# Optimization experiments

Hardware: AMD Instinct MI355X
Metric: run time of the kernel (lower is better)

## Reference

```python
import jax, jax.numpy as jnp
import numpy as np

B, N, C, H = 16, 577, 768, 12
D = C // H
BETA = 1.0
KEEP_RATIO = 0.5


def setup_inputs() -> dict:
    key = jax.random.key(0)
    k0, k1, k2, k3 = jax.random.split(key, 4)
    x = jax.random.normal(k0, (B, N, C), dtype=jnp.float32)
    # UCB visit-count buffer, strictly positive as accumulated counts would be
    ucb_count_score = jax.random.uniform(k1, (H, N), dtype=jnp.float32) * 50.0 + 1.0
    Wqkv = jax.random.normal(k2, (3 * C, C), dtype=jnp.float32) * 0.02
    Wproj = jax.random.normal(k3, (C, C), dtype=jnp.float32) * 0.02
    bproj = jnp.zeros((C,), dtype=jnp.float32)
    counter = 60  # > 50 so pruning path is taken
    return {"x": x, "ucb_count_score": ucb_count_score, "Wqkv": Wqkv,
            "Wproj": Wproj, "bproj": bproj, "counter": counter}


def reference(x, ucb_count_score, Wqkv, Wproj, bproj, counter):
    # UCBAttention.forward with pruning_enabled=True, selection_mode='ucb',
    # ucb_update_enabled=True, exclude_cls=True, dropout=0 (eval).
    Bs, Ns, Cs = x.shape
    scale = D ** -0.5
    k_keep = max(1, int((Ns - 1) * KEEP_RATIO))  # _get_k with keep_ratio

    qkv = (x @ Wqkv.T).reshape(Bs, Ns, 3, H, D).transpose(2, 0, 3, 1, 4)  # [3,B,H,N,D]
    q, k, v = qkv[0], qkv[1], qkv[2]
    attn_scores = jnp.einsum('bhqd,bhkd->bhqk', q, k) * scale
    attn_probs = jax.nn.softmax(attn_scores, axis=-1)  # [B,H,N,N]

    # UCB scores over patches (CLS excluded)
    patch_scores = attn_probs[:, :, :, 1:].mean(axis=2)            # [B,H,N-1]
    expl = BETA * jnp.sqrt(jnp.log(counter + 1.0) / (ucb_count_score[:, 1:] + 1e-6))
    ucb_scores = patch_scores + expl[None, :, :]                   # [B,H,N-1]
    global_ucb = ucb_scores.mean(axis=1)                           # [B,N-1]
    _, topk_rel = jax.lax.top_k(global_ucb, k_keep)                # [B,k]
    kept = topk_rel + 1                                            # token indices

    # keep-vector: CLS (0) always kept; mask[i,j] = kept[i] OR kept[j]
    kv_mask = (jnp.zeros((Bs, Ns), attn_probs.dtype)
               .at[jnp.arange(Bs)[:, None], kept].set(1.0)
               .at[:, 0].set(1.0))                                 # [B,N]
    mask = jnp.maximum(kv_mask[:, None, :, None], kv_mask[:, None, None, :])  # [B,1,N,N]

    pruned = attn_probs * mask
    pruned = pruned / (pruned.sum(axis=-1, keepdims=True) + 1e-8)
    context = jnp.einsum('bhqk,bhkd->bhqd', pruned, v)             # [B,H,N,D]

    out = context.transpose(0, 2, 1, 3).reshape(Bs, Ns, Cs) @ Wproj.T + bproj

    # score_delta: +1/B at each kept token column, broadcast over heads
    delta = jnp.zeros((Ns,), jnp.float32).at[kept.reshape(-1)].add(1.0 / Bs)
    score_delta = jnp.broadcast_to(delta[None, :], ucb_count_score.shape)
    return out, score_delta, kept
```

## Files before the change

### kernel.cpp

```cpp
#include <hip/hip_runtime.h>
#include <cstdio>
#include <cstdint>

#define B_    16
#define N_    577
#define C_    768
#define H_    12
#define D_    64
#define KKEEP 288
#define SCALE 0.125f
#define LOG2E 1.4426950408889634f
#define M_TOT (B_ * N_)
#define NKT   24
#define PLROW ((size_t)N_ * 64)

typedef __bf16 bf16x8_t __attribute__((ext_vector_type(8)));
typedef __bf16 bf16x4_t __attribute__((ext_vector_type(4)));
typedef float  f32x4_t  __attribute__((ext_vector_type(4)));
typedef unsigned int u32x4_t __attribute__((ext_vector_type(4)));
typedef unsigned int u32x2_t __attribute__((ext_vector_type(2)));

__device__ __forceinline__ f32x4_t mfma_bf16(bf16x8_t a, bf16x8_t b, f32x4_t c) {
    return __builtin_amdgcn_mfma_f32_16x16x32_bf16(a, b, c, 0, 0, 0);
}

__device__ __forceinline__ void gload16(const ushort* g, ushort* l) {
    __builtin_amdgcn_global_load_lds(
        (const __attribute__((address_space(1))) void*)g,
        (__attribute__((address_space(3))) void*)l, 16, 0, 0);
}
#define VMCNT(n) asm volatile("s_waitcnt vmcnt(" #n ")" ::: "memory")
#define SB() __builtin_amdgcn_sched_barrier(0)

__device__ __forceinline__ int xcd_swz(int bid, int nwg) {
    int q = nwg >> 3, r = nwg & 7;
    int xcd = bid & 7, off = bid >> 3;
    int base = (xcd < r) ? xcd * (q + 1) : r * (q + 1) + (xcd - r) * q;
    return base + off;
}

__device__ __forceinline__ void splitf(float x, unsigned int &hi, unsigned int &lo) {
    unsigned int u = __float_as_uint(x);
    hi = u >> 16;
    float r = x - __uint_as_float(u & 0xffff0000u);
    lo = __float_as_uint(r) >> 16;
}
__device__ __forceinline__ unsigned int bf16rne(float x) {
    unsigned int u = __float_as_uint(x);
    return (u + 0x7fffu + ((u >> 16) & 1u)) >> 16;
}

__global__ __launch_bounds__(256) void pack_tiles_kernel(const float* __restrict__ src,
                                                         ushort* __restrict__ dH,
                                                         ushort* __restrict__ dL,
                                                         int nrows) {
    int tile = blockIdx.x;
    int kt = tile % NKT, mt = tile / NKT;
    int w = threadIdx.x;
    int row = w >> 1, h = w & 1;
    int m = mt * 128 + row;
    int sw = (row >> 1) & 3;
    float f[16];
    if (m < nrows) {
        const float* s = src + (size_t)m * C_ + kt * 32;
        int sa = (2 * h) ^ sw, sb = (2 * h + 1) ^ sw;
        *(float4*)&f[0]  = *(const float4*)(s + sa * 8);
        *(float4*)&f[4]  = *(const float4*)(s + sa * 8 + 4);
        *(float4*)&f[8]  = *(const float4*)(s + sb * 8);
        *(float4*)&f[12] = *(const float4*)(s + sb * 8 + 4);
    } else {
#pragma unroll
        for (int i = 0; i < 16; i++) f[i] = 0.f;
    }
    unsigned hi[16], lo[16];
#pragma unroll
    for (int i = 0; i < 16; i++) splitf(f[i], hi[i], lo[i]);
    u32x4_t h0 = {hi[0] | (hi[1] << 16), hi[2] | (hi[3] << 16),
                  hi[4] | (hi[5] << 16), hi[6] | (hi[7] << 16)};
    u32x4_t h1 = {hi[8] | (hi[9] << 16), hi[10] | (hi[11] << 16),
                  hi[12] | (hi[13] << 16), hi[14] | (hi[15] << 16)};
    u32x4_t l0 = {lo[0] | (lo[1] << 16), lo[2] | (lo[3] << 16),
                  lo[4] | (lo[5] << 16), lo[6] | (lo[7] << 16)};
    u32x4_t l1 = {lo[8] | (lo[9] << 16), lo[10] | (lo[11] << 16),
                  lo[12] | (lo[13] << 16), lo[14] | (lo[15] << 16)};
    size_t dbase = (size_t)tile * 4096 + row * 32;
    *(u32x4_t*)&dH[dbase + (2 * h) * 8]     = h0;
    *(u32x4_t*)&dH[dbase + (2 * h + 1) * 8] = h1;
    *(u32x4_t*)&dL[dbase + (2 * h) * 8]     = l0;
    *(u32x4_t*)&dL[dbase + (2 * h + 1) * 8] = l1;
}

__global__ __launch_bounds__(256) void pack_rne_kernel(const float* __restrict__ src,
                                                       ushort* __restrict__ dst, int n8) {
    int i = blockIdx.x * 256 + threadIdx.x;
    if (i >= n8) return;
    float4 f0 = ((const float4*)src)[2 * i];
    float4 f1 = ((const float4*)src)[2 * i + 1];
    u32x4_t o = {bf16rne(f0.x) | (bf16rne(f0.y) << 16),
                 bf16rne(f0.z) | (bf16rne(f0.w) << 16),
                 bf16rne(f1.x) | (bf16rne(f1.y) << 16),
                 bf16rne(f1.z) | (bf16rne(f1.w) << 16)};
    *(u32x4_t*)&dst[(size_t)i * 8] = o;
}

__device__ __forceinline__ bf16x8_t fragT(const ushort* H, int row, int c, int ls) {
    int phys = ((c << 2) + ls) ^ (row & 7);
    return __builtin_bit_cast(bf16x8_t, *(const u32x4_t*)&H[(row << 6) + (phys << 3)]);
}

__global__ __launch_bounds__(256) void gemm_qk_mfma(const ushort* __restrict__ XplH,
                                                    const ushort* __restrict__ XplL,
                                                    const ushort* __restrict__ WplH,
                                                    const ushort* __restrict__ WplL,
                                                    ushort* __restrict__ qhp,
                                                    ushort* __restrict__ qlp,
                                                    ushort* __restrict__ khp,
                                                    ushort* __restrict__ klp) {
    __shared__ ushort SMEM[32768];
    ushort* Ah = SMEM;
    ushort* Al = SMEM + 8192;
    ushort* Bh = SMEM + 16384;
    ushort* Bl = SMEM + 24576;
    const int bid = xcd_swz(blockIdx.x, 12 * 73);
    const int bx = bid % 12, by = bid / 12;
    const int tid = threadIdx.x;
    const int lane = tid & 63, wave = tid >> 6;
    const int wr = wave >> 1, wc = wave & 1;
    const int lr = lane & 15, ls = lane >> 4;
    const int m0 = by * 128, n0 = bx * 128;
    const int s = n0 / C_;
    const int o0 = wave * 1024, o1 = o0 + 512;
    const int la = lane * 8;
    const size_t abase = (size_t)by * NKT * 4096;
    const size_t bbase = (size_t)bx * NKT * 4096;
    f32x4_t acc[4][4] = {};

    auto stage = [&](int buf, int kt) {
        const size_t ta = abase + (size_t)kt * 4096;
        const size_t tb = bbase + (size_t)kt * 4096;
        gload16(XplH + ta + o0 + la, &Ah[buf * 4096 + o0]);
        gload16(XplH + ta + o1 + la, &Ah[buf * 4096 + o1]);
        gload16(XplL + ta + o0 + la, &Al[buf * 4096 + o0]);
        gload16(XplL + ta + o1 + la, &Al[buf * 4096 + o1]);
        gload16(WplH + tb + o0 + la, &Bh[buf * 4096 + o0]);
        gload16(WplH + tb + o1 + la, &Bh[buf * 4096 + o1]);
        gload16(WplL + tb + o0 + la, &Bl[buf * 4096 + o0]);
        gload16(WplL + tb + o1 + la, &Bl[buf * 4096 + o1]);
    };
    stage(0, 0);
#pragma unroll 1
    for (int kt = 0; kt < NKT; ++kt) {
        const int cur = kt & 1;
        if (kt + 1 < NKT) {
            stage(cur ^ 1, kt + 1);
            VMCNT(8);
        } else {
            VMCNT(0);
        }
        SB();
        __builtin_amdgcn_s_barrier();
        SB();
        bf16x8_t fah[4], fal[4], fbh[4], fbl[4];
#pragma unroll
        for (int i = 0; i < 4; i++) {
            int rowA = wr * 64 + i * 16 + lr;
            int pa = ls ^ ((rowA >> 1) & 3);
            fah[i] = __builtin_bit_cast(bf16x8_t, *(const u32x4_t*)&Ah[cur * 4096 + rowA * 32 + pa * 8]);
            fal[i] = __builtin_bit_cast(bf16x8_t, *(const u32x4_t*)&Al[cur * 4096 + rowA * 32 + pa * 8]);
            int rowB = wc * 64 + i * 16 + lr;
            int pb = ls ^ ((rowB >> 1) & 3);
            fbh[i] = __builtin_bit_cast(bf16x8_t, *(const u32x4_t*)&Bh[cur * 4096 + rowB * 32 + pb * 8]);
            fbl[i] = __builtin_bit_cast(bf16x8_t, *(const u32x4_t*)&Bl[cur * 4096 + rowB * 32 + pb * 8]);
        }
#pragma unroll
        for (int i = 0; i < 4; i++)
#pragma unroll
            for (int j = 0; j < 4; j++) {
                acc[i][j] = mfma_bf16(fah[i], fbh[j], acc[i][j]);
                acc[i][j] = mfma_bf16(fah[i], fbl[j], acc[i][j]);
                acc[i][j] = mfma_bf16(fal[i], fbh[j], acc[i][j]);
            }
        if (kt + 1 < NKT) {
            SB();
            __builtin_amdgcn_s_barrier();
        }
    }
    __syncthreads();
    unsigned* T = (unsigned*)SMEM;
    const float sc = (s == 0) ? SCALE * LOG2E : 1.0f;
#pragma unroll
    for (int j = 0; j < 4; j++) {
        int nl = wc * 64 + j * 16 + lr;
#pragma unroll
        for (int i = 0; i < 4; i++) {
#pragma unroll
            for (int r = 0; r < 4; r++) {
                int ml = wr * 64 + i * 16 + ls * 4 + r;
                unsigned hi, lo;
                splitf(acc[i][j][r] * sc, hi, lo);
                int idx = ml * 128 + ((((nl >> 3) ^ (ml & 7)) << 3) | (nl & 7));
                T[idx] = hi | (lo << 16);
            }
        }
    }
    __syncthreads();
    ushort* dh = (s == 1) ? khp : qhp;
    ushort* dl = (s == 1) ? klp : qlp;
    const int hh0 = (n0 % C_) / D_;
#pragma unroll
    for (int it = 0; it < 8; ++it) {
        int g = it * 256 + tid;
        int sl = g & 7;
        int m_local = (g >> 3) & 127;
        int hh_half = g >> 10;
        int m = m0 + m_local;
        if (m < M_TOT) {
            int b = m / N_, n = m % N_;
            int dg = sl ^ (n & 7);
            int grp = (hh_half * 8 + dg) ^ (m_local & 7);
            const unsigned* src = &T[m_local * 128 + grp * 8];
            u32x4_t a = *(const u32x4_t*)src;
            u32x4_t bvv = *(const u32x4_t*)(src + 4);
            u32x4_t hiv = {(a[0] & 0xffffu) | (a[1] << 16),
                           (a[2] & 0xffffu) | (a[3] << 16),
                           (bvv[0] & 0xffffu) | (bvv[1] << 16),
                           (bvv[2] & 0xffffu) | (bvv[3] << 16)};
            u32x4_t lov = {(a[0] >> 16) | (a[1] & 0xffff0000u),
                           (a[2] >> 16) | (a[3] & 0xffff0000u),
                           (bvv[0] >> 16) | (bvv[1] & 0xffff0000u),
                           (bvv[2] >> 16) | (bvv[3] & 0xffff0000u)};
            size_t off = (size_t)(b * H_ + hh0 + hh_half) * PLROW + (size_t)n * 64 + sl * 8;
            *(u32x4_t*)&dh[off] = hiv;
            *(u32x4_t*)&dl[off] = lov;
        }
    }
}

__global__ __launch_bounds__(256) void gemm_v_mfma(const ushort* __restrict__ XplH,
                                                   const ushort* __restrict__ XplL,
                                                   const ushort* __restrict__ WplH,
                                                   ushort* __restrict__ vtp) {
    __shared__ ushort Ah[2][4096], Al[2][4096], Bh[2][4096];
    const int bid = xcd_swz(blockIdx.x, 6 * 73);
    const int bx = bid % 6, by = bid / 6;
    const int tid = threadIdx.x;
    const int lane = tid & 63, wave = tid >> 6;
    const int wr = wave >> 1, wc = wave & 1;
    const int lr = lane & 15, ls = lane >> 4;
    const int m0 = by * 128, n0v = bx * 128;
    const int o0 = wave * 1024, o1 = o0 + 512;
    const int la = lane * 8;
    const size_t abase = (size_t)by * NKT * 4096;
    const size_t bbase = (size_t)(12 + bx) * NKT * 4096;
    f32x4_t acc[4][4] = {};

    auto stage = [&](int buf, int kt) {
        const size_t ta = abase + (size_t)kt * 4096;
        const size_t tb = bbase + (size_t)kt * 4096;
        gload16(XplH + ta + o0 + la, &Ah[buf][o0]);
        gload16(XplH + ta + o1 + la, &Ah[buf][o1]);
        gload16(XplL + ta + o0 + la, &Al[buf][o0]);
        gload16(XplL + ta + o1 + la, &Al[buf][o1]);
        gload16(WplH + tb + o0 + la, &Bh[buf][o0]);
        gload16(WplH + tb + o1 + la, &Bh[buf][o1]);
    };
    stage(0, 0);
#pragma unroll 1
    for (int kt = 0; kt < NKT; ++kt) {
        const int cur = kt & 1;
        if (kt + 1 < NKT) {
            stage(cur ^ 1, kt + 1);
            VMCNT(6);
        } else {
            VMCNT(0);
        }
        SB();
        __builtin_amdgcn_s_barrier();
        SB();
        bf16x8_t fah[4], fal[4], fbh[4];
#pragma unroll
        for (int i = 0; i < 4; i++) {
            int rowA = wr * 64 + i * 16 + lr;
            int pa = ls ^ ((rowA >> 1) & 3);
            fah[i] = __builtin_bit_cast(bf16x8_t, *(const u32x4_t*)&Ah[cur][rowA * 32 + pa * 8]);
            fal[i] = __builtin_bit_cast(bf16x8_t, *(const u32x4_t*)&Al[cur][rowA * 32 + pa * 8]);
            int rowB = wc * 64 + i * 16 + lr;
            int pb = ls ^ ((rowB >> 1) & 3);
            fbh[i] = __builtin_bit_cast(bf16x8_t, *(const u32x4_t*)&Bh[cur][rowB * 32 + pb * 8]);
        }
#pragma unroll
        for (int i = 0; i < 4; i++)
#pragma unroll
            for (int j = 0; j < 4; j++) {
                acc[i][j] = mfma_bf16(fah[i], fbh[j], acc[i][j]);
                acc[i][j] = mfma_bf16(fal[i], fbh[j], acc[i][j]);
            }
        if (kt + 1 < NKT) {
            SB();
            __builtin_amdgcn_s_barrier();
        }
    }
#pragma unroll
    for (int j = 0; j < 4; j++) {
        int ng = n0v + wc * 64 + j * 16 + lr;
        int hh = ng / D_;
        int d = ng % D_;
#pragma unroll
        for (int i = 0; i < 4; i++) {
            int mg0 = m0 + wr * 64 + i * 16 + ls * 4;
#pragma unroll
            for (int r = 0; r < 4; r++) {
                int m = mg0 + r;
                if (m < M_TOT) {
                    int b = m / N_, n = m % N_;
                    int jt = n >> 6, jl = n & 63;
                    size_t off = ((size_t)(b * H_ + hh) * 10 + jt) * 4096 +
                                 (size_t)d * 64 + (((jl >> 3) ^ (d & 7)) << 3) + (jl & 7);
                    vtp[off] = __builtin_bit_cast(unsigned short, (__bf16)acc[i][j][r]);
                }
            }
        }
    }
}

__global__ __launch_bounds__(512) void attn_rowsum_mfma(const ushort* __restrict__ qh,
                                                        const ushort* __restrict__ ql,
                                                        const ushort* __restrict__ kh,
                                                        const ushort* __restrict__ kl,
                                                        float* __restrict__ w) {
    __shared__ ushort Qh[8192], Ql[8192];
    __shared__ ushort Kh[2][4096], Kl[2][4096];
    __shared__ float red[8][64];
    const int bid = xcd_swz(blockIdx.x, 5 * B_ * H_);
    const int bh = bid / 5, q0 = (bid % 5) * 128;
    const int tid = threadIdx.x, lane = tid & 63, wv = tid >> 6;
    const int wg = wv >> 2, wl = wv & 3;
    const int lr = lane & 15, ls = lane >> 4;
    const size_t bho = (size_t)bh * PLROW;
    const ushort* qhp = qh + bho; const ushort* qlp = ql + bho;
    const ushort* khp = kh + bho; const ushort* klp = kl + bho;
    auto qrow = [&](int rr) { return (size_t)min(q0 + wv * 16 + rr * 8 + (lane >> 3), N_ - 1) * 64 + (lane & 7) * 8; };
    gload16(qhp + qrow(0), &Qh[wv * 1024]);
    gload16(qhp + qrow(1), &Qh[wv * 1024 + 512]);
    gload16(qlp + qrow(0), &Ql[wv * 1024]);
    gload16(qlp + qrow(1), &Ql[wv * 1024 + 512]);
    auto krow = [&](int j0) { return (size_t)min(j0 + wv * 8 + (lane >> 3), N_ - 1) * 64 + (lane & 7) * 8; };
    auto stageK = [&](int buf, int j0) {
        gload16(khp + krow(j0), &Kh[buf][wv * 512]);
        gload16(klp + krow(j0), &Kl[buf][wv * 512]);
    };
    VMCNT(0);
    __syncthreads();
    bf16x8_t fqh[4][2], fql[4][2];
#pragma unroll
    for (int i = 0; i < 4; i++)
#pragma unroll
        for (int c = 0; c < 2; c++) {
            fqh[i][c] = fragT(Qh, wg * 64 + i * 16 + lr, c, ls);
            fql[i][c] = fragT(Ql, wg * 64 + i * 16 + lr, c, ls);
        }
    stageK(0, 0);
    float rs[4] = {0.f, 0.f, 0.f, 0.f};
#pragma unroll 1
    for (int t = 0; t < 10; ++t) {
        const int cur = t & 1;
        if (t < 9) { stageK(cur ^ 1, (t + 1) * 64); VMCNT(2); }
        else      { VMCNT(0); }
        SB(); __builtin_amdgcn_s_barrier(); SB();
        bf16x8_t fkh[2], fkl[2];
#pragma unroll
        for (int c = 0; c < 2; c++) {
            fkh[c] = fragT(Kh[cur], wl * 16 + lr, c, ls);
            fkl[c] = fragT(Kl[cur], wl * 16 + lr, c, ls);
        }
        int jbase = t * 64 + wl * 16 + ls * 4;
#pragma unroll
        for (int i = 0; i < 4; i++) {
            f32x4_t s = {0.f, 0.f, 0.f, 0.f};
            __builtin_amdgcn_s_setprio(1);
#pragma unroll
            for (int c = 0; c < 2; c++) {
                s = mfma_bf16(fkh[c], fqh[i][c], s);
                s = mfma_bf16(fkh[c], fql[i][c], s);
                s = mfma_bf16(fkl[c], fqh[i][c], s);
            }
            __builtin_amdgcn_s_setprio(0);
#pragma unroll
            for (int r = 0; r < 4; r++)
                rs[i] += (jbase + r < N_) ? __builtin_amdgcn_exp2f(s[r]) : 0.f;
        }
        if (t < 9) { SB(); __builtin_amdgcn_s_barrier(); }
    }
#pragma unroll
    for (int i = 0; i < 4; i++) {
        float v2 = rs[i];
        v2 += __shfl_xor(v2, 16);
        v2 += __shfl_xor(v2, 32);
        if (ls == 0) red[wv][i * 16 + lr] = v2;
    }
    __syncthreads();
    if (tid < 128) {
        int grp = tid >> 6, qlc = tid & 63;
        float s = red[grp * 4 + 0][qlc] + red[grp * 4 + 1][qlc] +
                  red[grp * 4 + 2][qlc] + red[grp * 4 + 3][qlc];
        int qn = q0 + tid;
        if (qn < N_) w[(size_t)bh * N_ + qn] = 1.0f / s;
    }
}

__global__ __launch_bounds__(512) void attn_colsum_mfma(const ushort* __restrict__ qh,
                                                        const ushort* __restrict__ ql,
                                                        const ushort* __restrict__ kh,
                                                        const ushort* __restrict__ kl,
                                                        const float* __restrict__ w,
                                                        float* __restrict__ colsum) {
    __shared__ ushort KhS[8192], KlS[8192];
    __shared__ ushort Qh[2][4096], Ql[2][4096];
    __shared__ float wsAll[640];
    __shared__ float red[8][64];
    const int bid = xcd_swz(blockIdx.x, 5 * B_ * H_);
    const int bh = bid / 5, j0 = (bid % 5) * 128;
    const int tid = threadIdx.x, lane = tid & 63, wv = tid >> 6;
    const int wg = wv >> 2, wl = wv & 3;
    const int lr = lane & 15, ls = lane >> 4;
    const size_t bho = (size_t)bh * PLROW;
    const ushort* qhp = qh + bho; const ushort* qlp = ql + bho;
    const ushort* khp = kh + bho; const ushort* klp = kl + bho;
    auto krow = [&](int rr) { return (size_t)min(j0 + wv * 16 + rr * 8 + (lane >> 3), N_ - 1) * 64 + (lane & 7) * 8; };
    gload16(khp + krow(0), &KhS[wv * 1024]);
    gload16(khp + krow(1), &KhS[wv * 1024 + 512]);
    gload16(klp + krow(0), &KlS[wv * 1024]);
    gload16(klp + krow(1), &KlS[wv * 1024 + 512]);
    for (int i2 = tid; i2 < 640; i2 += 512)
        wsAll[i2] = (i2 < N_) ? w[(size_t)bh * N_ + i2] : 0.f;
    auto qrow = [&](int qt) { return (size_t)min(qt + wv * 8 + (lane >> 3), N_ - 1) * 64 + (lane & 7) * 8; };
    auto stageQ = [&](int buf, int qt) {
        gload16(qhp + qrow(qt), &Qh[buf][wv * 512]);
        gload16(qlp + qrow(qt), &Ql[buf][wv * 512]);
    };
    VMCNT(0);
    __syncthreads();
    bf16x8_t fkh[4][2], fkl[4][2];
#pragma unroll
    for (int i = 0; i < 4; i++)
#pragma unroll
        for (int c = 0; c < 2; c++) {
            fkh[i][c] = fragT(KhS, wg * 64 + i * 16 + lr, c, ls);
            fkl[i][c] = fragT(KlS, wg * 64 + i * 16 + lr, c, ls);
        }
    stageQ(0, 0);
    float cs[4] = {0.f, 0.f, 0.f, 0.f};
#pragma unroll 1
    for (int t = 0; t < 10; ++t) {
        const int cur = t & 1;
        if (t < 9) { stageQ(cur ^ 1, (t + 1) * 64); VMCNT(2); }
        else      { VMCNT(0); }
        SB(); __builtin_amdgcn_s_barrier(); SB();
        bf16x8_t fqh[2], fql[2];
#pragma unroll
        for (int c = 0; c < 2; c++) {
            fqh[c] = fragT(Qh[cur], wl * 16 + lr, c, ls);
            fql[c] = fragT(Ql[cur], wl * 16 + lr, c, ls);
        }
        float wq[4];
#pragma unroll
        for (int r = 0; r < 4; r++) wq[r] = wsAll[t * 64 + wl * 16 + ls * 4 + r];
#pragma unroll
        for (int i = 0; i < 4; i++) {
            f32x4_t s = {0.f, 0.f, 0.f, 0.f};
            __builtin_amdgcn_s_setprio(1);
#pragma unroll
            for (int c = 0; c < 2; c++) {
                s = mfma_bf16(fqh[c], fkh[i][c], s);
                s = mfma_bf16(fql[c], fkh[i][c], s);
                s = mfma_bf16(fqh[c], fkl[i][c], s);
            }
            __builtin_amdgcn_s_setprio(0);
#pragma unroll
            for (int r = 0; r < 4; r++) cs[i] += __builtin_amdgcn_exp2f(s[r]) * wq[r];
        }
        if (t < 9) { SB(); __builtin_amdgcn_s_barrier(); }
    }
#pragma unroll
    for (int i = 0; i < 4; i++) {
        float v2 = cs[i];
        v2 += __shfl_xor(v2, 16);
        v2 += __shfl_xor(v2, 32);
        if (ls == 0) red[wv][i * 16 + lr] = v2;
    }
    __syncthreads();
    if (tid < 128) {
        int grp = tid >> 6, jlc = tid & 63;
        float t2 = red[grp * 4 + 0][jlc] + red[grp * 4 + 1][jlc] +
                   red[grp * 4 + 2][jlc] + red[grp * 4 + 3][jlc];
        int jn = j0 + tid;
        if (jn < N_) colsum[(size_t)bh * N_ + jn] = t2;
    }
}

__global__ __launch_bounds__(512) void topk_kernel(const float* __restrict__ colsum,
                                                   const float* __restrict__ ucb_count,
                                                   const int* __restrict__ counter,
                                                   float* __restrict__ kept_out,
                                                   float* __restrict__ kvmask) {
    __shared__ float sv[1024];
    __shared__ int si[1024];
    int b = blockIdx.x, tid = threadIdx.x;
    float lc = logf((float)counter[0] + 1.0f);
    for (int t = tid; t < 1024; t += 512) {
        if (t < N_ - 1) {
            int tok = t + 1;
            float accv = 0.f;
#pragma unroll
            for (int h = 0; h < H_; h++) {
                float csv = colsum[(size_t)(b * H_ + h) * N_ + tok];
                float patch = csv * (1.0f / (float)N_);
                float cnt = ucb_count[h * N_ + tok];
                float expl = sqrtf(lc / (cnt + 1e-6f));
                accv += patch + expl;
            }
            sv[t] = accv * (1.0f / (float)H_);
            si[t] = t;
        } else {
            sv[t] = -INFINITY;
            si[t] = 1 << 20;
        }
    }
    __syncthreads();
    for (int kk = 2; kk <= 1024; kk <<= 1) {
        for (int jj = kk >> 1; jj > 0; jj >>= 1) {
            for (int t = tid; t < 1024; t += 512) {
                int ixj = t ^ jj;
                if (ixj > t) {
                    float v1 = sv[t], v2 = sv[ixj];
                    int i1 = si[t], i2 = si[ixj];
                    bool before21 = (v2 > v1) || (v2 == v1 && i2 < i1);
                    bool dirDesc = ((t & kk) == 0);
                    if (before21 == dirDesc) {
                        sv[t] = v2; sv[ixj] = v1;
                        si[t] = i2; si[ixj] = i1;
                    }
                }
            }
            __syncthreads();
        }
    }
    for (int r = tid; r < KKEEP; r += 512) {
        int tok = si[r] + 1;
        kept_out[b * KKEEP + r] = (float)tok;
        kvmask[b * N_ + tok] = 1.0f;
    }
    if (tid == 0) kvmask[b * N_] = 1.0f;
}

__global__ void score_delta_kernel(const float* __restrict__ kvmask,
                                   float* __restrict__ sd) {
    int idx = blockIdx.x * 256 + threadIdx.x;
    if (idx >= H_ * N_) return;
    int n = idx % N_;
    float d = 0.f;
    if (n != 0) {
#pragma unroll
        for (int b = 0; b < B_; b++) d += kvmask[b * N_ + n];
    }
    sd[idx] = d * (1.0f / (float)B_);
}

__global__ __launch_bounds__(512) void attn_ctx_mfma(const ushort* __restrict__ qh,
                                                     const ushort* __restrict__ ql,
                                                     const ushort* __restrict__ kh,
                                                     const ushort* __restrict__ kl,
                                                     const ushort* __restrict__ vtp,
                                                     const float* __restrict__ w,
                                                     const float* __restrict__ kvmask,
                                                     ushort* __restrict__ ctxb) {
    __shared__ ushort Kh[2][4096], Kl[2][4096], Vt[2][4096];
    __shared__ ushort Pl[2][4096];
    __shared__ float wsAll[640], mkAll[640], red[8][64], inv[128];
    const int bid = xcd_swz(blockIdx.x, 5 * B_ * H_);
    const int bh = bid / 5, q0 = (bid % 5) * 128;
    const int b = bh / H_, h = bh % H_;
    const int tid = threadIdx.x, lane = tid & 63, wv = tid >> 6;
    const int wg = wv >> 2, wl = wv & 3;
    const int lr = lane & 15, ls = lane >> 4;
    const size_t bho = (size_t)bh * PLROW;
    const ushort* qhp = qh + bho; const ushort* qlp = ql + bho;
    const ushort* khp = kh + bho; const ushort* klp = kl + bho;
    const ushort* vtb = vtp + (size_t)bh * 10 * 4096;
    ushort* PlS = &Pl[0][0];
    for (int i2 = tid; i2 < 640; i2 += 512) {
        wsAll[i2] = (i2 < N_) ? w[(size_t)bh * N_ + i2] : 0.f;
        mkAll[i2] = (i2 < N_) ? kvmask[(size_t)b * N_ + i2] : 0.f;
    }
    auto qrow = [&](int rr) { return (size_t)min(q0 + wv * 16 + rr * 8 + (lane >> 3), N_ - 1) * 64 + (lane & 7) * 8; };
    bf16x8_t fqh[4][2], fql[4][2];
    gload16(qhp + qrow(0), &PlS[wv * 1024]);
    gload16(qhp + qrow(1), &PlS[wv * 1024 + 512]);
    VMCNT(0); __syncthreads();
#pragma unroll
    for (int i = 0; i < 4; i++)
#pragma unroll
        for (int c = 0; c < 2; c++)
            fqh[i][c] = fragT(PlS, wg * 64 + i * 16 + lr, c, ls);
    __syncthreads();
    gload16(qlp + qrow(0), &PlS[wv * 1024]);
    gload16(qlp + qrow(1), &PlS[wv * 1024 + 512]);
    VMCNT(0); __syncthreads();
#pragma unroll
    for (int i = 0; i < 4; i++)
#pragma unroll
        for (int c = 0; c < 2; c++)
            fql[i][c] = fragT(PlS, wg * 64 + i * 16 + lr, c, ls);
    __syncthreads();
    auto krow = [&](int j0) { return (size_t)min(j0 + wv * 8 + (lane >> 3), N_ - 1) * 64 + (lane & 7) * 8; };
    auto stageKV = [&](int buf, int t) {
        int j0 = t * 64;
        gload16(khp + krow(j0), &Kh[buf][wv * 512]);
        gload16(klp + krow(j0), &Kl[buf][wv * 512]);
        gload16(vtb + (size_t)t * 4096 + wv * 512 + lane * 8, &Vt[buf][wv * 512]);
    };
    float wq[4], mq[4];
#pragma unroll
    for (int i = 0; i < 4; i++) {
        wq[i] = wsAll[q0 + wg * 64 + i * 16 + lr];
        mq[i] = mkAll[q0 + wg * 64 + i * 16 + lr];
    }
    stageKV(0, 0);
    f32x4_t acc[4] = {};
    float psums[4] = {0.f, 0.f, 0.f, 0.f};
#pragma unroll 1
    for (int t = 0; t < 10; ++t) {
        const int cur = t & 1;
        if (t < 9) { stageKV(cur ^ 1, t + 1); VMCNT(3); }
        else      { VMCNT(0); }
        SB(); __builtin_amdgcn_s_barrier(); SB();
        bf16x8_t fkh[2], fkl[2];
#pragma unroll
        for (int c = 0; c < 2; c++) {
            fkh[c] = fragT(Kh[cur], wl * 16 + lr, c, ls);
            fkl[c] = fragT(Kl[cur], wl * 16 + lr, c, ls);
        }
        int jloc = wl * 16 + ls * 4;
#pragma unroll
        for (int i = 0; i < 4; i++) {
            f32x4_t s = {0.f, 0.f, 0.f, 0.f};
            __builtin_amdgcn_s_setprio(1);
#pragma unroll
            for (int c = 0; c < 2; c++) {
                s = mfma_bf16(fkh[c], fqh[i][c], s);
                s = mfma_bf16(fkh[c], fql[i][c], s);
                s = mfma_bf16(fkl[c], fqh[i][c], s);
            }
            __builtin_amdgcn_s_setprio(0);
            bf16x4_t pb;
            float wqi = wq[i], mqi = mq[i];
#pragma unroll
            for (int r = 0; r < 4; r++) {
                int j = t * 64 + jloc + r;
                float mj = mkAll[jloc + t * 64 + r];
                float p = (j < N_) ? __builtin_amdgcn_exp2f(s[r]) * wqi : 0.f;
                p = (mqi > 0.5f || mj > 0.5f) ? p : 0.f;
                psums[i] += p;
                pb[r] = (__bf16)p;
            }
            int row = i * 16 + lr;
            int slot = ((wl << 1) + (ls >> 1)) ^ (row & 7);
            *(u32x2_t*)&Pl[wg][(row << 6) + (slot << 3) + ((ls & 1) << 2)] =
                __builtin_bit_cast(u32x2_t, pb);
        }
        __syncthreads();
        bf16x8_t fv[2];
#pragma unroll
        for (int c = 0; c < 2; c++) fv[c] = fragT(Vt[cur], wl * 16 + lr, c, ls);
        __builtin_amdgcn_s_setprio(1);
#pragma unroll
        for (int i = 0; i < 4; i++) {
            bf16x8_t fp0 = fragT(Pl[wg], i * 16 + lr, 0, ls);
            bf16x8_t fp1 = fragT(Pl[wg], i * 16 + lr, 1, ls);
            acc[i] = mfma_bf16(fv[0], fp0, acc[i]);
            acc[i] = mfma_bf16(fv[1], fp1, acc[i]);
        }
        __builtin_amdgcn_s_setprio(0);
        if (t < 9) { SB(); __builtin_amdgcn_s_barrier(); }
    }
#pragma unroll
    for (int i = 0; i < 4; i++) {
        float v2 = psums[i];
        v2 += __shfl_xor(v2, 16);
        v2 += __shfl_xor(v2, 32);
        if (ls == 0) red[wv][i * 16 + lr] = v2;
    }
    __syncthreads();
    if (tid < 128) {
        int grp = tid >> 6, qlc = tid & 63;
        float t2 = red[grp * 4 + 0][qlc] + red[grp * 4 + 1][qlc] +
                   red[grp * 4 + 2][qlc] + red[grp * 4 + 3][qlc];
        inv[tid] = 1.0f / (t2 + 1e-8f);
    }
    __syncthreads();
#pragma unroll
    for (int i = 0; i < 4; i++) {
        int qn = q0 + wg * 64 + i * 16 + lr;
        if (qn < N_) {
            float rn = inv[wg * 64 + i * 16 + lr];
            bf16x4_t ov;
            ov[0] = (__bf16)(acc[i][0] * rn);
            ov[1] = (__bf16)(acc[i][1] * rn);
            ov[2] = (__bf16)(acc[i][2] * rn);
            ov[3] = (__bf16)(acc[i][3] * rn);
            *(u32x2_t*)&ctxb[((size_t)(b * N_ + qn)) * C_ + h * D_ + wl * 16 + ls * 4] =
                __builtin_bit_cast(u32x2_t, ov);
        }
    }
}

__global__ __launch_bounds__(256) void gemm_proj_mfma(const ushort* __restrict__ Actx,
                                                      const ushort* __restrict__ Wb,
                                                      const float* __restrict__ bias,
                                                      float* __restrict__ out) {
    __shared__ ushort Ab[128 * 32], Bb[128 * 32];
    const int bid = xcd_swz(blockIdx.x, 6 * 73);
    const int bx = bid % 6, by = bid / 6;
    const int tid = threadIdx.x;
    const int lane = tid & 63, wave = tid >> 6;
    const int wr = wave >> 1, wc = wave & 1;
    const int lr = lane & 15, ls = lane >> 4;
    const int m0 = by * 128, n0 = bx * 128;
    const int srow = tid >> 1, shalf = tid & 1;
    const int arow = min(m0 + srow, M_TOT - 1);
    const ushort* aptr = Actx + (size_t)arow * C_ + shalf * 16;
    const ushort* bptr = Wb + (size_t)(n0 + srow) * C_ + shalf * 16;
    const int swz = (srow >> 1) & 3;
    const int sidx = srow * 32;
    const int p0 = (shalf * 2 + 0) ^ swz, p1 = (shalf * 2 + 1) ^ swz;
    f32x4_t acc[4][4] = {};
#pragma unroll 1
    for (int k0 = 0; k0 < C_; k0 += 32) {
        __syncthreads();
        {
            u32x4_t c0 = *(const u32x4_t*)(aptr + k0);
            u32x4_t c1 = *(const u32x4_t*)(aptr + k0 + 8);
            *(u32x4_t*)&Ab[sidx + p0 * 8] = c0;
            *(u32x4_t*)&Ab[sidx + p1 * 8] = c1;
        }
        {
            u32x4_t c0 = *(const u32x4_t*)(bptr + k0);
            u32x4_t c1 = *(const u32x4_t*)(bptr + k0 + 8);
            *(u32x4_t*)&Bb[sidx + p0 * 8] = c0;
            *(u32x4_t*)&Bb[sidx + p1 * 8] = c1;
        }
        __syncthreads();
        bf16x8_t fa[4], fb[4];
#pragma unroll
        for (int i = 0; i < 4; i++) {
            int rowA = wr * 64 + i * 16 + lr;
            int pa = ls ^ ((rowA >> 1) & 3);
            fa[i] = __builtin_bit_cast(bf16x8_t, *(const u32x4_t*)&Ab[rowA * 32 + pa * 8]);
            int rowB = wc * 64 + i * 16 + lr;
            int pb = ls ^ ((rowB >> 1) & 3);
            fb[i] = __builtin_bit_cast(bf16x8_t, *(const u32x4_t*)&Bb[rowB * 32 + pb * 8]);
        }
#pragma unroll
        for (int i = 0; i < 4; i++)
#pragma unroll
            for (int j = 0; j < 4; j++)
                acc[i][j] = mfma_bf16(fa[i], fb[j], acc[i][j]);
    }
#pragma unroll
    for (int j = 0; j < 4; j++) {
        int ng = n0 + wc * 64 + j * 16 + lr;
        float bb = bias[ng];
#pragma unroll
        for (int i = 0; i < 4; i++) {
            int mg0 = m0 + wr * 64 + i * 16 + ls * 4;
#pragma unroll
            for (int r = 0; r < 4; r++) {
                int m = mg0 + r;
                if (m < M_TOT) out[(size_t)m * C_ + ng] = acc[i][j][r] + bb;
            }
        }
    }
}

extern "C" void kernel_launch(void* const* d_in, const int* in_sizes, int n_in,
                              void* d_out, int out_size, void* d_ws, size_t ws_size,
                              hipStream_t stream) {
    const float* x     = (const float*)d_in[0];
    const float* ucb   = (const float*)d_in[1];
    const float* Wqkv  = (const float*)d_in[2];
    const float* Wproj = (const float*)d_in[3];
    const float* bproj = (const float*)d_in[4];
    const int*   counter = (const int*)d_in[5];

    const size_t BHN  = (size_t)B_ * H_ * N_;
    const size_t XPL  = (size_t)(73 * 128) * C_;
    const size_t WPL  = (size_t)3 * C_ * C_;
    const size_t WPJ  = (size_t)C_ * C_;
    const size_t PLN  = (size_t)192 * PLROW;
    const size_t VTSZ = (size_t)192 * 10 * 4096;

    ushort* qhp  = (ushort*)d_ws;
    ushort* qlp  = qhp + PLN;
    ushort* khp  = qlp + PLN;
    ushort* klp  = khp + PLN;
    ushort* vtp  = klp + PLN;
    ushort* XplH = vtp + VTSZ;
    ushort* XplL = XplH + XPL;
    ushort* ctxb = XplH;
    ushort* WplH = XplL + XPL;
    ushort* WplL = WplH + WPL;
    ushort* Wpjb = WplL + WPL;
    float*  w    = (float*)(Wpjb + WPJ);
    float*  colsum = w + BHN;
    float*  kvmask = colsum + BHN;
    size_t need = ((char*)(kvmask + (size_t)B_ * N_)) - (char*)d_ws;
    if (ws_size < need) {
        fprintf(stderr, "kernel_launch: ws too small, need %zu have %zu\n",
                need, ws_size);
        return;
    }

    float* out  = (float*)d_out;
    float* sd   = out + (size_t)B_ * N_ * C_;
    float* kept = sd + (size_t)H_ * N_;

    hipMemsetAsync(kvmask, 0, (size_t)B_ * N_ * sizeof(float), stream);

    pack_tiles_kernel<<<73 * NKT, 256, 0, stream>>>(x, XplH, XplL, M_TOT);
    pack_tiles_kernel<<<18 * NKT, 256, 0, stream>>>(Wqkv, WplH, WplL, 3 * C_);
    pack_rne_kernel<<<(int)(WPJ / 8 / 256), 256, 0, stream>>>(Wproj, Wpjb, (int)(WPJ / 8));

    gemm_qk_mfma<<<12 * 73, 256, 0, stream>>>(XplH, XplL, WplH, WplL,
                                              qhp, qlp, khp, klp);
    gemm_v_mfma<<<6 * 73, 256, 0, stream>>>(XplH, XplL, WplH, vtp);
    attn_rowsum_mfma<<<5 * B_ * H_, 512, 0, stream>>>(qhp, qlp, khp, klp, w);
    attn_colsum_mfma<<<5 * B_ * H_, 512, 0, stream>>>(qhp, qlp, khp, klp, w, colsum);
    topk_kernel<<<B_, 512, 0, stream>>>(colsum, ucb, counter, kept, kvmask);
    score_delta_kernel<<<(H_ * N_ + 255) / 256, 256, 0, stream>>>(kvmask, sd);
    attn_ctx_mfma<<<5 * B_ * H_, 512, 0, stream>>>(qhp, qlp, khp, klp, vtp,
                                                   w, kvmask, ctxb);
    gemm_proj_mfma<<<6 * 73, 256, 0, stream>>>(ctxb, Wpjb, bproj, out);
}
```

Measured before the change: 318.7 us.

## Single-buffer Q/K staging in row/col sums and drop redundant row scaling in ctx

The rowsum and colsum attention kernels go from double-buffered to single-buffered K/Q tiles in LDS. Each tile is now loaded between two barriers with a full wait. This cuts LDS per block so more blocks can be resident per CU, but it gives up the overlap of the next tile's load with the current tile's compute. The context kernel stops multiplying by the per-row softmax reciprocal w, since that factor cancels in the later renormalisation by the pruned row sum. It also replaces the column-bound and mask branches with a large negative exponent bias and an fmax of the masks, and uses an lgkmcnt wait plus a raw barrier instead of __syncthreads.

New measurement: 319.2 us. No clear change (+0.1%).

```diff
diff --git a/kernel.cpp b/kernel.cpp
--- a/kernel.cpp
+++ b/kernel.cpp
@@ -30,6 +30,7 @@
         (__attribute__((address_space(3))) void*)l, 16, 0, 0);
 }
 #define VMCNT(n) asm volatile("s_waitcnt vmcnt(" #n ")" ::: "memory")
+#define LGKM0()  asm volatile("s_waitcnt lgkmcnt(0)" ::: "memory")
 #define SB() __builtin_amdgcn_sched_barrier(0)
 
 __device__ __forceinline__ int xcd_swz(int bid, int nwg) {
@@ -329,7 +330,7 @@
                                                         const ushort* __restrict__ kl,
                                                         float* __restrict__ w) {
     __shared__ ushort Qh[8192], Ql[8192];
-    __shared__ ushort Kh[2][4096], Kl[2][4096];
+    __shared__ ushort Kh[4096], Kl[4096];
     __shared__ float red[8][64];
     const int bid = xcd_swz(blockIdx.x, 5 * B_ * H_);
     const int bh = bid / 5, q0 = (bid % 5) * 128;
@@ -345,10 +346,11 @@
     gload16(qlp + qrow(0), &Ql[wv * 1024]);
     gload16(qlp + qrow(1), &Ql[wv * 1024 + 512]);
     auto krow = [&](int j0) { return (size_t)min(j0 + wv * 8 + (lane >> 3), N_ - 1) * 64 + (lane & 7) * 8; };
-    auto stageK = [&](int buf, int j0) {
-        gload16(khp + krow(j0), &Kh[buf][wv * 512]);
-        gload16(klp + krow(j0), &Kl[buf][wv * 512]);
+    auto stageK = [&](int j0) {
+        gload16(khp + krow(j0), &Kh[wv * 512]);
+        gload16(klp + krow(j0), &Kl[wv * 512]);
     };
+    stageK(0);
     VMCNT(0);
     __syncthreads();
     bf16x8_t fqh[4][2], fql[4][2];
@@ -359,19 +361,14 @@
             fqh[i][c] = fragT(Qh, wg * 64 + i * 16 + lr, c, ls);
             fql[i][c] = fragT(Ql, wg * 64 + i * 16 + lr, c, ls);
         }
-    stageK(0, 0);
     float rs[4] = {0.f, 0.f, 0.f, 0.f};
 #pragma unroll 1
     for (int t = 0; t < 10; ++t) {
-        const int cur = t & 1;
-        if (t < 9) { stageK(cur ^ 1, (t + 1) * 64); VMCNT(2); }
-        else      { VMCNT(0); }
-        SB(); __builtin_amdgcn_s_barrier(); SB();
         bf16x8_t fkh[2], fkl[2];
 #pragma unroll
         for (int c = 0; c < 2; c++) {
-            fkh[c] = fragT(Kh[cur], wl * 16 + lr, c, ls);
-            fkl[c] = fragT(Kl[cur], wl * 16 + lr, c, ls);
+            fkh[c] = fragT(Kh, wl * 16 + lr, c, ls);
+            fkl[c] = fragT(Kl, wl * 16 + lr, c, ls);
         }
         int jbase = t * 64 + wl * 16 + ls * 4;
 #pragma unroll
@@ -389,7 +386,12 @@
             for (int r = 0; r < 4; r++)
                 rs[i] += (jbase + r < N_) ? __builtin_amdgcn_exp2f(s[r]) : 0.f;
         }
-        if (t < 9) { SB(); __builtin_amdgcn_s_barrier(); }
+        if (t < 9) {
+            SB(); __builtin_amdgcn_s_barrier(); SB();
+            stageK((t + 1) * 64);
+            VMCNT(0);
+            SB(); __builtin_amdgcn_s_barrier(); SB();
+        }
     }
 #pragma unroll
     for (int i = 0; i < 4; i++) {
@@ -415,7 +417,7 @@
                                                         const float* __restrict__ w,
                                                         float* __restrict__ colsum) {
     __shared__ ushort KhS[8192], KlS[8192];
-    __shared__ ushort Qh[2][4096], Ql[2][4096];
+    __shared__ ushort Qh[4096], Ql[4096];
     __shared__ float wsAll[640];
     __shared__ float red[8][64];
     const int bid = xcd_swz(blockIdx.x, 5 * B_ * H_);
@@ -431,13 +433,14 @@
     gload16(khp + krow(1), &KhS[wv * 1024 + 512]);
     gload16(klp + krow(0), &KlS[wv * 1024]);
     gload16(klp + krow(1), &KlS[wv * 1024 + 512]);
+    auto qrow2 = [&](int qt) { return (size_t)min(qt + wv * 8 + (lane >> 3), N_ - 1) * 64 + (lane & 7) * 8; };
+    auto stageQ = [&](int qt) {
+        gload16(qhp + qrow2(qt), &Qh[wv * 512]);
+        gload16(qlp + qrow2(qt), &Ql[wv * 512]);
+    };
+    stageQ(0);
     for (int i2 = tid; i2 < 640; i2 += 512)
         wsAll[i2] = (i2 < N_) ? w[(size_t)bh * N_ + i2] : 0.f;
-    auto qrow = [&](int qt) { return (size_t)min(qt + wv * 8 + (lane >> 3), N_ - 1) * 64 + (lane & 7) * 8; };
-    auto stageQ = [&](int buf, int qt) {
-        gload16(qhp + qrow(qt), &Qh[buf][wv * 512]);
-        gload16(qlp + qrow(qt), &Ql[buf][wv * 512]);
-    };
     VMCNT(0);
     __syncthreads();
     bf16x8_t fkh[4][2], fkl[4][2];
@@ -448,19 +451,14 @@
             fkh[i][c] = fragT(KhS, wg * 64 + i * 16 + lr, c, ls);
             fkl[i][c] = fragT(KlS, wg * 64 + i * 16 + lr, c, ls);
         }
-    stageQ(0, 0);
     float cs[4] = {0.f, 0.f, 0.f, 0.f};
 #pragma unroll 1
     for (int t = 0; t < 10; ++t) {
-        const int cur = t & 1;
-        if (t < 9) { stageQ(cur ^ 1, (t + 1) * 64); VMCNT(2); }
-        else      { VMCNT(0); }
-        SB(); __builtin_amdgcn_s_barrier(); SB();
         bf16x8_t fqh[2], fql[2];
 #pragma unroll
         for (int c = 0; c < 2; c++) {
-            fqh[c] = fragT(Qh[cur], wl * 16 + lr, c, ls);
-            fql[c] = fragT(Ql[cur], wl * 16 + lr, c, ls);
+            fqh[c] = fragT(Qh, wl * 16 + lr, c, ls);
+            fql[c] = fragT(Ql, wl * 16 + lr, c, ls);
         }
         float wq[4];
 #pragma unroll
@@ -479,7 +477,12 @@
 #pragma unroll
             for (int r = 0; r < 4; r++) cs[i] += __builtin_amdgcn_exp2f(s[r]) * wq[r];
         }
-        if (t < 9) { SB(); __builtin_amdgcn_s_barrier(); }
+        if (t < 9) {
+            SB(); __builtin_amdgcn_s_barrier(); SB();
+            stageQ((t + 1) * 64);
+            VMCNT(0);
+            SB(); __builtin_amdgcn_s_barrier(); SB();
+        }
     }
 #pragma unroll
     for (int i = 0; i < 4; i++) {
@@ -571,12 +574,11 @@
                                                      const ushort* __restrict__ kh,
                                                      const ushort* __restrict__ kl,
                                                      const ushort* __restrict__ vtp,
-                                                     const float* __restrict__ w,
                                                      const float* __restrict__ kvmask,
                                                      ushort* __restrict__ ctxb) {
     __shared__ ushort Kh[2][4096], Kl[2][4096], Vt[2][4096];
     __shared__ ushort Pl[2][4096];
-    __shared__ float wsAll[640], mkAll[640], red[8][64], inv[128];
+    __shared__ float mkAll[640], red[8][64], inv[128];
     const int bid = xcd_swz(blockIdx.x, 5 * B_ * H_);
     const int bh = bid / 5, q0 = (bid % 5) * 128;
     const int b = bh / H_, h = bh % H_;
@@ -588,10 +590,8 @@
     const ushort* khp = kh + bho; const ushort* klp = kl + bho;
     const ushort* vtb = vtp + (size_t)bh * 10 * 4096;
     ushort* PlS = &Pl[0][0];
-    for (int i2 = tid; i2 < 640; i2 += 512) {
-        wsAll[i2] = (i2 < N_) ? w[(size_t)bh * N_ + i2] : 0.f;
+    for (int i2 = tid; i2 < 640; i2 += 512)
         mkAll[i2] = (i2 < N_) ? kvmask[(size_t)b * N_ + i2] : 0.f;
-    }
     auto qrow = [&](int rr) { return (size_t)min(q0 + wv * 16 + rr * 8 + (lane >> 3), N_ - 1) * 64 + (lane & 7) * 8; };
     bf16x8_t fqh[4][2], fql[4][2];
     gload16(qhp + qrow(0), &PlS[wv * 1024]);
@@ -619,12 +619,9 @@
         gload16(klp + krow(j0), &Kl[buf][wv * 512]);
         gload16(vtb + (size_t)t * 4096 + wv * 512 + lane * 8, &Vt[buf][wv * 512]);
     };
-    float wq[4], mq[4];
-#pragma unroll
-    for (int i = 0; i < 4; i++) {
-        wq[i] = wsAll[q0 + wg * 64 + i * 16 + lr];
-        mq[i] = mkAll[q0 + wg * 64 + i * 16 + lr];
-    }
+    float mq[4];
+#pragma unroll
+    for (int i = 0; i < 4; i++) mq[i] = mkAll[q0 + wg * 64 + i * 16 + lr];
     stageKV(0, 0);
     f32x4_t acc[4] = {};
     float psums[4] = {0.f, 0.f, 0.f, 0.f};
@@ -641,6 +638,13 @@
             fkl[c] = fragT(Kl[cur], wl * 16 + lr, c, ls);
         }
         int jloc = wl * 16 + ls * 4;
+        float jmv[4], jbias[4];
+#pragma unroll
+        for (int r = 0; r < 4; r++) {
+            int j = t * 64 + jloc + r;
+            jmv[r] = mkAll[t * 64 + jloc + r];
+            jbias[r] = (j < N_) ? 0.f : -16384.f;
+        }
 #pragma unroll
         for (int i = 0; i < 4; i++) {
             f32x4_t s = {0.f, 0.f, 0.f, 0.f};
@@ -653,13 +657,10 @@
             }
             __builtin_amdgcn_s_setprio(0);
             bf16x4_t pb;
-            float wqi = wq[i], mqi = mq[i];
+            float mqi = mq[i];
 #pragma unroll
             for (int r = 0; r < 4; r++) {
-                int j = t * 64 + jloc + r;
-                float mj = mkAll[jloc + t * 64 + r];
-                float p = (j < N_) ? __builtin_amdgcn_exp2f(s[r]) * wqi : 0.f;
-                p = (mqi > 0.5f || mj > 0.5f) ? p : 0.f;
+                float p = __builtin_amdgcn_exp2f(s[r] + jbias[r]) * fmaxf(mqi, jmv[r]);
                 psums[i] += p;
                 pb[r] = (__bf16)p;
             }
@@ -668,7 +669,9 @@
             *(u32x2_t*)&Pl[wg][(row << 6) + (slot << 3) + ((ls & 1) << 2)] =
                 __builtin_bit_cast(u32x2_t, pb);
         }
-        __syncthreads();
+        SB(); LGKM0(); SB();
+        __builtin_amdgcn_s_barrier();
+        SB();
         bf16x8_t fv[2];
 #pragma unroll
         for (int c = 0; c < 2; c++) fv[c] = fragT(Vt[cur], wl * 16 + lr, c, ls);
@@ -838,6 +841,6 @@
     topk_kernel<<<B_, 512, 0, stream>>>(colsum, ucb, counter, kept, kvmask);
     score_delta_kernel<<<(H_ * N_ + 255) / 256, 256, 0, stream>>>(kvmask, sd);
     attn_ctx_mfma<<<5 * B_ * H_, 512, 0, stream>>>(qhp, qlp, khp, klp, vtp,
-                                                   w, kvmask, ctxb);
+                                                   kvmask, ctxb);
     gemm_proj_mfma<<<6 * 73, 256, 0, stream>>>(ctxb, Wpjb, bproj, out);
 }
```
